# Kernel optimization log

Measured on AMD Instinct MI355X. Metric: run time of the kernel, lower is better.

## Reference

```python
import math
import jax, jax.numpy as jnp
import numpy as np

S = 2048      # seq_length
D = 1024      # embedding_dim
H = 16        # num_qkv_heads
HD = D // H   # head_size = 64
L = 4         # num_hidden_layers
V = 32000     # vocab_size
EPS = 1e-5    # nn.LayerNorm default eps


def setup_inputs() -> dict:
    key = jax.random.key(0)
    ks = jax.random.split(key, 16)
    def n(k, shape, scale=0.02):
        return (jax.random.normal(k, shape, jnp.float32) * scale)
    return {
        "input_ids": jax.random.randint(ks[0], (S,), 0, V),
        "embed":     n(ks[1], (V, D)),
        "pos_enc":   n(ks[2], (S, D)),
        # per-layer stacked params; nn.Linear stores W as [out, in]
        "wq": n(ks[3], (L, D, D)), "bq": jnp.zeros((L, D), jnp.float32),
        "wk": n(ks[4], (L, D, D)), "bk": jnp.zeros((L, D), jnp.float32),
        "wv": n(ks[5], (L, D, D)), "bv": jnp.zeros((L, D), jnp.float32),
        "wo": n(ks[6], (L, D, D)), "bo": jnp.zeros((L, D), jnp.float32),
        "ln1_g": jnp.ones((L, D), jnp.float32), "ln1_b": jnp.zeros((L, D), jnp.float32),
        "w1": n(ks[7], (L, 4 * D, D)), "b1": jnp.zeros((L, 4 * D), jnp.float32),
        "w2": n(ks[8], (L, D, 4 * D)), "b2": jnp.zeros((L, D), jnp.float32),
        "ln2_g": jnp.ones((L, D), jnp.float32), "ln2_b": jnp.zeros((L, D), jnp.float32),
        "lm_head": n(ks[9], (V, D)),
    }


def _layer_norm(x, g, b):
    mu = jnp.mean(x, axis=-1, keepdims=True)
    var = jnp.mean(jnp.square(x - mu), axis=-1, keepdims=True)
    return (x - mu) * jax.lax.rsqrt(var + EPS) * g + b


def _forward(input_ids, embed, pos_enc, wq, bq, wk, bk, wv, bv, wo, bo,
             ln1_g, ln1_b, w1, b1, w2, b2, ln2_g, ln2_b, lm_head):
    s = input_ids.shape[0]
    h = embed[input_ids] + pos_enc[:s]                      # [S, D]
    causal = jnp.tril(jnp.ones((s, s), dtype=bool))         # [S, S]
    inv_sqrt_dk = 1.0 / math.sqrt(HD)

    def layer(h, p):
        (lwq, lbq, lwk, lbk, lwv, lbv, lwo, lbo,
         g1, bn1, lw1, lb1, lw2, lb2, g2, bn2) = p
        q = (h @ lwq.T + lbq).reshape(s, H, HD).transpose(1, 0, 2)  # [H, S, HD]
        k = (h @ lwk.T + lbk).reshape(s, H, HD).transpose(1, 0, 2)
        v = (h @ lwv.T + lbv).reshape(s, H, HD).transpose(1, 0, 2)
        scores = jnp.einsum('hqd,hkd->hqk', q, k) * inv_sqrt_dk     # [H, S, S]
        scores = jnp.where(causal, scores, -jnp.inf)
        attn = jax.nn.softmax(scores, axis=-1)
        o = jnp.einsum('hqk,hkd->hqd', attn, v)                     # [H, S, HD]
        o = o.transpose(1, 0, 2).reshape(s, D) @ lwo.T + lbo        # [S, D]
        h = _layer_norm(h + o, g1, bn1)
        m = jax.nn.relu(h @ lw1.T + lb1) @ lw2.T + lb2              # [S, D]
        h = _layer_norm(h + m, g2, bn2)
        return h, None

    h, _ = jax.lax.scan(layer, h, (wq, bq, wk, bk, wv, bv, wo, bo,
                                   ln1_g, ln1_b, w1, b1, w2, b2, ln2_g, ln2_b))
    return h @ lm_head.T                                    # [S, V] logits


def reference(input_ids, embed, pos_enc, wq, bq, wk, bk, wv, bv, wo, bo,
              ln1_g, ln1_b, w1, b1, w2, b2, ln2_g, ln2_b, lm_head):
    return _forward(input_ids, embed, pos_enc, wq, bq, wk, bk, wv, bv, wo, bo,
                    ln1_g, ln1_b, w1, b1, w2, b2, ln2_g, ln2_b, lm_head)
```

## Files before the change

kernel.cpp:

```cpp
#include <hip/hip_runtime.h>
#include <hip/hip_bf16.h>

#define S 2048
#define D 1024
#define NH 16
#define HD 64
#define NL 4
#define VOCAB 32000
#define DFF 4096
#define EPS_LN 1e-5f

typedef unsigned short ushortT;
typedef __attribute__((ext_vector_type(8))) short short8;
typedef __attribute__((ext_vector_type(4))) unsigned short ushort4v;
typedef __attribute__((ext_vector_type(4))) float f32x4;

__device__ __forceinline__ ushortT f2bf(float f) {
    unsigned u = __float_as_uint(f);
    u += 0x7FFFu + ((u >> 16) & 1u);
    return (ushortT)(u >> 16);
}

__device__ __forceinline__ void gload_lds16(const ushortT* g, ushortT* l) {
    auto gp = (const __attribute__((address_space(1))) unsigned int*)(uintptr_t)g;
    auto lp = (__attribute__((address_space(3))) unsigned int*)(uintptr_t)l;
    __builtin_amdgcn_global_load_lds(gp, lp, 16, 0, 0);
}

__device__ __forceinline__ void cvt8(const float* s, ushortT* d) {
    float4 a = *(const float4*)s;
    float4 b = *(const float4*)(s + 4);
    short8 r;
    r[0] = (short)f2bf(a.x); r[1] = (short)f2bf(a.y);
    r[2] = (short)f2bf(a.z); r[3] = (short)f2bf(a.w);
    r[4] = (short)f2bf(b.x); r[5] = (short)f2bf(b.y);
    r[6] = (short)f2bf(b.z); r[7] = (short)f2bf(b.w);
    *(short8*)d = r;
}

__global__ __launch_bounds__(256) void embed_kernel(
    const int* __restrict__ ids, const float* __restrict__ embed,
    const float* __restrict__ pos, float* __restrict__ hf, ushortT* __restrict__ hb)
{
    int i = blockIdx.x * 256 + threadIdx.x;
    int srow = i >> 10;
    int d = i & (D - 1);
    float v = embed[(size_t)ids[srow] * D + d] + pos[i];
    hf[i] = v;
    hb[i] = f2bf(v);
}

__global__ __launch_bounds__(256) void convert_layer(
    const float* __restrict__ wq, const float* __restrict__ wk, const float* __restrict__ wv,
    const float* __restrict__ wo, const float* __restrict__ w1, const float* __restrict__ w2,
    const float* __restrict__ bq, const float* __restrict__ bk, const float* __restrict__ bv,
    int l, ushortT* __restrict__ wl, float* __restrict__ bqkv)
{
    constexpr int R = (D * D) / 8;
    const int u = blockIdx.x * 256 + threadIdx.x;
    if (u < 12 * R) {
        const float* src;
        if (u < 3 * R) {
            int sub = u >> 17, off = u & (R - 1);
            const float* w = (sub == 0) ? wq : (sub == 1) ? wk : wv;
            src = w + (size_t)l * D * D + (size_t)off * 8;
        } else if (u < 4 * R) {
            src = wo + (size_t)l * D * D + (size_t)(u - 3 * R) * 8;
        } else if (u < 8 * R) {
            src = w1 + (size_t)l * 4 * D * D + (size_t)(u - 4 * R) * 8;
        } else {
            src = w2 + (size_t)l * 4 * D * D + (size_t)(u - 8 * R) * 8;
        }
        cvt8(src, wl + (size_t)u * 8);
    } else if (u < 12 * R + 384) {
        int i = u - 12 * R;
        int sub = i >> 7, off = (i & 127) * 8;
        const float* src = ((sub == 0) ? bq : (sub == 1) ? bk : bv) + (size_t)l * D + off;
        *(float4*)(bqkv + sub * D + off)     = *(const float4*)src;
        *(float4*)(bqkv + sub * D + off + 4) = *(const float4*)(src + 4);
    }
}

__global__ __launch_bounds__(256) void convert_flat(
    const float* __restrict__ src, ushortT* __restrict__ dst)
{
    const size_t u = (size_t)blockIdx.x * 256 + threadIdx.x;
    cvt8(src + u * 8, dst + u * 8);
}

template<int BN, int OUTMODE, int RELU, int HASBIAS>
__global__ __launch_bounds__(256) void gemm_bf(
    const ushortT* __restrict__ A, const ushortT* __restrict__ B,
    const float* __restrict__ bias, void* __restrict__ Cn, void* __restrict__ Ct,
    int N, int K)
{
    constexpr int WN = BN / 2;
    constexpr int NCT = WN / 16;
    __shared__ alignas(16) ushortT As[128 * 32];
    __shared__ alignas(16) ushortT Bs[BN * 32];

    const int tid = threadIdx.x;
    const int id = blockIdx.x;
    const int brow = (id & 15) * 128;
    const int bcol = (id >> 4) * BN;
    const int lane = tid & 63, wid = tid >> 6;
    const int l15 = lane & 15, l4 = lane >> 4;
    const int wr = wid >> 1, wc = wid & 1;
    const int str = tid >> 2;
    const int stc = (tid & 3) * 8;

    f32x4 acc[4][NCT] = {};

    const ushortT* Ab = A + (size_t)(brow + str) * K + stc;
    const ushortT* Bb = B + (size_t)(bcol + str) * K + stc;
    ushortT* AsD = &As[tid * 8];
    ushortT* BsD = &Bs[tid * 8];

    const int nkb = K >> 5;
    for (int kb = 0; kb < nkb; ++kb) {
        const int ko = kb * 32;
        gload_lds16(Ab + ko, AsD);
        gload_lds16(Ab + ko + (size_t)64 * K, AsD + 2048);
        gload_lds16(Bb + ko, BsD);
        if (BN == 128) gload_lds16(Bb + ko + (size_t)64 * K, BsD + 2048);
        __syncthreads();

        short8 af[4], bfr[NCT];
        #pragma unroll
        for (int rt = 0; rt < 4; ++rt)
            af[rt] = *(const short8*)&As[(wr * 64 + rt * 16 + l15) * 32 + l4 * 8];
        #pragma unroll
        for (int ct = 0; ct < NCT; ++ct)
            bfr[ct] = *(const short8*)&Bs[(wc * WN + ct * 16 + l15) * 32 + l4 * 8];
        #pragma unroll
        for (int rt = 0; rt < 4; ++rt)
            #pragma unroll
            for (int ct = 0; ct < NCT; ++ct)
                acc[rt][ct] = __builtin_amdgcn_mfma_f32_16x16x32_bf16(af[rt], bfr[ct], acc[rt][ct], 0, 0, 0);
        __syncthreads();
    }

    #pragma unroll
    for (int rt = 0; rt < 4; ++rt) {
        const int crow0 = brow + wr * 64 + rt * 16 + l4 * 4;
        #pragma unroll
        for (int ct = 0; ct < NCT; ++ct) {
            const int ccol = bcol + wc * WN + ct * 16 + l15;
            const float bv = HASBIAS ? bias[ccol] : 0.0f;
            if (OUTMODE == 0) {
                float* C = (float*)Cn;
                #pragma unroll
                for (int j = 0; j < 4; ++j) {
                    float v = acc[rt][ct][j] + bv;
                    if (RELU) v = fmaxf(v, 0.0f);
                    C[(size_t)(crow0 + j) * N + ccol] = v;
                }
            } else if (OUTMODE == 1) {
                ushortT* C = (ushortT*)Cn;
                #pragma unroll
                for (int j = 0; j < 4; ++j) {
                    float v = acc[rt][ct][j] + bv;
                    if (RELU) v = fmaxf(v, 0.0f);
                    C[(size_t)(crow0 + j) * N + ccol] = f2bf(v);
                }
            }
        }
    }
}

template<int OUTMODE, int RELU, int HASBIAS>
__global__ __launch_bounds__(512) void gemm256(
    const ushortT* __restrict__ A, const ushortT* __restrict__ B,
    const float* __restrict__ bias, void* __restrict__ Cn, void* __restrict__ Ct,
    int N, int K)
{
    __shared__ alignas(128) ushortT lds[65536];

    const int tid = threadIdx.x;
    const int NB = N >> 8;
    const int bid = blockIdx.x;
    const int wgid = (bid & 7) * NB + (bid >> 3);
    const int brow = (wgid & 7) << 8;
    const int bcol = (wgid >> 3) << 8;

    const int lane = tid & 63;
    const int wid = tid >> 6;
    const int l15 = lane & 15, l4 = lane >> 4;
    const int wm = wid >> 2, wn = wid & 3;

    const int NT = K >> 6;

    const int srow = tid >> 3;
    const int scol = ((tid & 7) ^ (srow & 7)) * 8;
    const ushortT* Asrc = A + (size_t)(brow + srow) * K + scol;
    const ushortT* Bsrc = B + (size_t)(bcol + srow) * K + scol;

    auto stA = [&](int t, int h) {
        if (t < NT) {
            const int bb = t & 1;
            #pragma unroll
            for (int g = 0; g < 2; ++g)
                gload_lds16(Asrc + (size_t)(h * 128 + g * 64) * K + (size_t)t * 64,
                            &lds[bb * 32768 + h * 8192 + g * 4096 + tid * 8]);
        }
    };
    auto stB = [&](int t, int h) {
        if (t < NT) {
            const int bb = t & 1;
            #pragma unroll
            for (int g = 0; g < 2; ++g)
                gload_lds16(Bsrc + (size_t)(h * 128 + g * 64) * K + (size_t)t * 64,
                            &lds[bb * 32768 + 16384 + h * 8192 + g * 4096 + tid * 8]);
        }
    };

    f32x4 acc[2][2][4][2] = {};

    stA(0, 0); stB(0, 0); stA(0, 1); stB(0, 1); stB(1, 0); stA(1, 0);
    asm volatile("s_waitcnt vmcnt(4)" ::: "memory");
    __builtin_amdgcn_s_barrier();

#define RD_A(DST, RC)                                                          \
    _Pragma("unroll") for (int r16 = 0; r16 < 4; ++r16)                        \
    _Pragma("unroll") for (int kk = 0; kk < 2; ++kk)                           \
        DST[r16][kk] = *(const short8*)&lds[b * 32768 +                        \
            (((RC) * 128 + wm * 64 + r16 * 16 + l15) << 6) +                   \
            ((((kk << 2) + l4) ^ (l15 & 7)) << 3)];
#define RD_B(DST, CC)                                                          \
    _Pragma("unroll") for (int c16 = 0; c16 < 2; ++c16)                        \
    _Pragma("unroll") for (int kk = 0; kk < 2; ++kk)                           \
        DST[c16][kk] = *(const short8*)&lds[b * 32768 + 16384 +                \
            (((CC) * 128 + wn * 32 + c16 * 16 + l15) << 6) +                   \
            ((((kk << 2) + l4) ^ (l15 & 7)) << 3)];
#define MFMA_Q(AF, BF, RC, CC)                                                 \
    __builtin_amdgcn_s_setprio(1);                                             \
    _Pragma("unroll") for (int kk = 0; kk < 2; ++kk)                           \
    _Pragma("unroll") for (int r16 = 0; r16 < 4; ++r16)                        \
    _Pragma("unroll") for (int c16 = 0; c16 < 2; ++c16)                        \
        acc[RC][CC][r16][c16] = __builtin_amdgcn_mfma_f32_16x16x32_bf16(       \
            AF[r16][kk], BF[c16][kk], acc[RC][CC][r16][c16], 0, 0, 0);         \
    __builtin_amdgcn_s_setprio(0);
#define WAIT_LGKM asm volatile("s_waitcnt lgkmcnt(0)" ::: "memory");

    for (int t = 0; t < NT; ++t) {
        const int b = t & 1;
        short8 a_[4][2], b0[2][2], b1[2][2];

        RD_A(a_, 0); RD_B(b0, 0);
        stA(t + 1, 1);
        asm volatile("s_waitcnt lgkmcnt(8)" ::: "memory");
        __builtin_amdgcn_s_barrier();
        WAIT_LGKM;
        MFMA_Q(a_, b0, 0, 0);
        __builtin_amdgcn_s_barrier();

        RD_B(b1, 1);
        stB(t + 1, 1);
        __builtin_amdgcn_s_barrier();
        WAIT_LGKM;
        MFMA_Q(a_, b1, 0, 1);
        __builtin_amdgcn_s_barrier();

        RD_A(a_, 1);
        stB(t + 2, 0);
        __builtin_amdgcn_s_barrier();
        WAIT_LGKM;
        MFMA_Q(a_, b1, 1, 1);
        __builtin_amdgcn_s_barrier();

        stA(t + 2, 0);
        __builtin_amdgcn_s_barrier();
        MFMA_Q(a_, b0, 1, 0);
        if (t < NT - 2) { asm volatile("s_waitcnt vmcnt(4)" ::: "memory"); }
        else            { asm volatile("s_waitcnt vmcnt(0)" ::: "memory"); }
        __builtin_amdgcn_s_barrier();
    }
#undef RD_A
#undef RD_B
#undef MFMA_Q
#undef WAIT_LGKM

    #pragma unroll
    for (int rc = 0; rc < 2; ++rc)
    #pragma unroll
    for (int cc = 0; cc < 2; ++cc)
    #pragma unroll
    for (int r16 = 0; r16 < 4; ++r16)
    #pragma unroll
    for (int c16 = 0; c16 < 2; ++c16) {
        const int crow0 = brow + rc * 128 + wm * 64 + r16 * 16 + l4 * 4;
        const int ccol  = bcol + cc * 128 + wn * 32 + c16 * 16 + l15;
        const float bv = HASBIAS ? bias[ccol] : 0.0f;
        if (OUTMODE == 0) {
            float* C = (float*)Cn;
            #pragma unroll
            for (int j = 0; j < 4; ++j) {
                float v = acc[rc][cc][r16][c16][j] + bv;
                if (RELU) v = fmaxf(v, 0.0f);
                __builtin_nontemporal_store(v, &C[(size_t)(crow0 + j) * N + ccol]);
            }
        } else if (OUTMODE == 1) {
            ushortT* C = (ushortT*)Cn;
            #pragma unroll
            for (int j = 0; j < 4; ++j) {
                float v = acc[rc][cc][r16][c16][j] + bv;
                if (RELU) v = fmaxf(v, 0.0f);
                C[(size_t)(crow0 + j) * N + ccol] = f2bf(v);
            }
        }
    }
}

template<int OUTMODE, int RELU, int HASBIAS, int SWAP>
__global__ __launch_bounds__(512) void gemm256v(
    const ushortT* __restrict__ A, const ushortT* __restrict__ B,
    const float* __restrict__ bias, void* __restrict__ Cn, void* __restrict__ Ct,
    int N, int NBn, int Kloop, int stride)
{
    __shared__ alignas(128) ushortT lds[73728];

    const int tid = threadIdx.x;
    const int bid = blockIdx.x;
    const int cpx = gridDim.x >> 3;
    const int wgid = (bid & 7) * cpx + (bid >> 3);
    const int brow = (wgid & 7) << 8;
    const int rest = wgid >> 3;
    const int split = rest / NBn;
    const int bcol = (rest - split * NBn) << 7;
    const int kofs = split * Kloop;

    const int lane = tid & 63, wid = tid >> 6;
    const int l15 = lane & 15, l4 = lane >> 4;
    const int wm = wid >> 1, wn = wid & 1;
    const int NT = Kloop >> 6;

    const int srow = tid >> 3;
    const int scol = ((tid & 7) ^ (srow & 7)) * 8;
    const ushortT* Asrc = A + (size_t)(brow + srow) * stride + kofs + scol;
    const ushortT* Bsrc = B + (size_t)(bcol + srow) * stride + kofs + scol;

    auto stA = [&](int t, int h) {
        if (t < NT) {
            const int sb = t % 3;
            #pragma unroll
            for (int g = 0; g < 2; ++g)
                gload_lds16(Asrc + (size_t)(h * 128 + g * 64) * stride + (size_t)t * 64,
                            &lds[sb * 24576 + h * 8192 + g * 4096 + tid * 8]);
        }
    };
    auto stB = [&](int t) {
        if (t < NT) {
            const int sb = t % 3;
            #pragma unroll
            for (int g = 0; g < 2; ++g)
                gload_lds16(Bsrc + (size_t)(g * 64) * stride + (size_t)t * 64,
                            &lds[sb * 24576 + 16384 + g * 4096 + tid * 8]);
        }
    };

    f32x4 acc[4][4] = {};

    stA(0, 0); stA(0, 1); stB(0);
    stA(1, 0); stA(1, 1); stB(1);
    asm volatile("s_waitcnt vmcnt(6)" ::: "memory");
    __builtin_amdgcn_s_barrier();

    for (int t = 0; t < NT; ++t) {
        const unsigned abase = (unsigned)(t % 3) * 24576;
        short8 af[4][2], bf2[2][2];

        #pragma unroll
        for (int r16 = 0; r16 < 4; ++r16)
            #pragma unroll
            for (int kk = 0; kk < 2; ++kk)
                af[r16][kk] = *(const short8*)&lds[abase +
                    ((wm * 64 + r16 * 16 + l15) << 6) +
                    ((((kk << 2) + l4) ^ (l15 & 7)) << 3)];
        #pragma unroll
        for (int c16 = 0; c16 < 2; ++c16)
            #pragma unroll
            for (int kk = 0; kk < 2; ++kk)
                bf2[c16][kk] = *(const short8*)&lds[abase + 16384 +
                    ((wn * 64 + c16 * 16 + l15) << 6) +
                    ((((kk << 2) + l4) ^ (l15 & 7)) << 3)];
        stA(t + 2, 0); stA(t + 2, 1);
        asm volatile("s_waitcnt lgkmcnt(8)" ::: "memory");
        __builtin_amdgcn_s_barrier();
        asm volatile("s_waitcnt lgkmcnt(0)" ::: "memory");
        __builtin_amdgcn_s_setprio(1);
        #pragma unroll
        for (int kk = 0; kk < 2; ++kk)
            #pragma unroll
            for (int r16 = 0; r16 < 4; ++r16)
                #pragma unroll
                for (int c16 = 0; c16 < 2; ++c16)
                    acc[r16][c16] = SWAP
                        ? __builtin_amdgcn_mfma_f32_16x16x32_bf16(bf2[c16][kk], af[r16][kk], acc[r16][c16], 0, 0, 0)
                        : __builtin_amdgcn_mfma_f32_16x16x32_bf16(af[r16][kk], bf2[c16][kk], acc[r16][c16], 0, 0, 0);
        __builtin_amdgcn_s_setprio(0);
        __builtin_amdgcn_s_barrier();

        #pragma unroll
        for (int c16 = 0; c16 < 2; ++c16)
            #pragma unroll
            for (int kk = 0; kk < 2; ++kk)
                bf2[c16][kk] = *(const short8*)&lds[abase + 16384 +
                    ((wn * 64 + (c16 + 2) * 16 + l15) << 6) +
                    ((((kk << 2) + l4) ^ (l15 & 7)) << 3)];
        stB(t + 2);
        __builtin_amdgcn_s_barrier();
        asm volatile("s_waitcnt lgkmcnt(0)" ::: "memory");
        __builtin_amdgcn_s_setprio(1);
        #pragma unroll
        for (int kk = 0; kk < 2; ++kk)
            #pragma unroll
            for (int r16 = 0; r16 < 4; ++r16)
                #pragma unroll
                for (int c16 = 0; c16 < 2; ++c16)
                    acc[r16][c16 + 2] = SWAP
                        ? __builtin_amdgcn_mfma_f32_16x16x32_bf16(bf2[c16][kk], af[r16][kk], acc[r16][c16 + 2], 0, 0, 0)
                        : __builtin_amdgcn_mfma_f32_16x16x32_bf16(af[r16][kk], bf2[c16][kk], acc[r16][c16 + 2], 0, 0, 0);
        __builtin_amdgcn_s_setprio(0);
        if (t + 2 < NT) { asm volatile("s_waitcnt vmcnt(6)" ::: "memory"); }
        else            { asm volatile("s_waitcnt vmcnt(0)" ::: "memory"); }
        __builtin_amdgcn_s_barrier();
    }

    #pragma unroll
    for (int r16 = 0; r16 < 4; ++r16)
    #pragma unroll
    for (int c16 = 0; c16 < 4; ++c16) {
        if (SWAP) {
            const int row = brow + wm * 64 + r16 * 16 + l15;
            const int col = bcol + wn * 64 + c16 * 16 + l4 * 4;
            f32x4 v = acc[r16][c16];
            if (HASBIAS) {
                float4 b4 = *(const float4*)&bias[col];
                v[0] += b4.x; v[1] += b4.y; v[2] += b4.z; v[3] += b4.w;
            }
            if (RELU) {
                #pragma unroll
                for (int j = 0; j < 4; ++j) v[j] = fmaxf(v[j], 0.0f);
            }
            if (OUTMODE == 1) {
                ushort4v o;
                #pragma unroll
                for (int j = 0; j < 4; ++j) o[j] = f2bf(v[j]);
                *(ushort4v*)&((ushortT*)Cn)[(size_t)row * N + col] = o;
            } else if (OUTMODE == 3) {
                float* C = (float*)Cn + (size_t)split * 2048 * N;
                *(f32x4*)&C[(size_t)row * N + col] = v;
            } else {
                __builtin_nontemporal_store(v, (f32x4*)&((float*)Cn)[(size_t)row * N + col]);
            }
        } else {
            const int crow0 = brow + wm * 64 + r16 * 16 + l4 * 4;
            const int ccol  = bcol + wn * 64 + c16 * 16 + l15;
            const float bv = HASBIAS ? bias[ccol] : 0.0f;
            if (OUTMODE == 2) {
                if (ccol < 2048) {
                    ushortT* C = (ushortT*)Cn;
                    #pragma unroll
                    for (int j = 0; j < 4; ++j)
                        C[(size_t)(crow0 + j) * 2048 + ccol] = f2bf(acc[r16][c16][j] + bv);
                } else {
                    ushortT* C = (ushortT*)Ct;
                    ushort4v wv_;
                    #pragma unroll
                    for (int j = 0; j < 4; ++j) wv_[j] = f2bf(acc[r16][c16][j] + bv);
                    *(ushort4v*)&C[(size_t)(ccol - 2048) * S + crow0] = wv_;
                }
            } else if (OUTMODE == 1) {
                ushortT* C = (ushortT*)Cn;
                #pragma unroll
                for (int j = 0; j < 4; ++j) {
                    float v = acc[r16][c16][j] + bv;
                    if (RELU) v = fmaxf(v, 0.0f);
                    C[(size_t)(crow0 + j) * N + ccol] = f2bf(v);
                }
            } else {
                float* C = (float*)Cn;
                #pragma unroll
                for (int j = 0; j < 4; ++j) {
                    float v = acc[r16][c16][j] + bv;
                    if (RELU) v = fmaxf(v, 0.0f);
                    C[(size_t)(crow0 + j) * N + ccol] = v;
                }
            }
        }
    }
}

__global__ __launch_bounds__(256) void attn_kernel(
    const ushortT* __restrict__ qk, const ushortT* __restrict__ vt,
    ushortT* __restrict__ att)
{
    const int h = blockIdx.y;
    const int q0 = blockIdx.x * 64;
    const int tid = threadIdx.x;
    const int w = tid >> 6, lane = tid & 63;
    const int l15 = lane & 15, l4 = lane >> 4;
    const int qrow0 = q0 + w * 16;

    __shared__ short p_lds[4][16][48];

    short8 aq[2];
    {
        const ushortT* qp = qk + (size_t)(qrow0 + l15) * 2048 + h * HD + l4 * 8;
        aq[0] = *(const short8*)qp;
        aq[1] = *(const short8*)(qp + 32);
    }

    f32x4 o[4] = {};
    float lsum[4] = {0.f, 0.f, 0.f, 0.f};

    const int nkb = blockIdx.x * 2 + 2;
    for (int kb32 = 0; kb32 < nkb; ++kb32) {
        const int kb = kb32 * 32;
        f32x4 s[2] = {};
        #pragma unroll
        for (int kh = 0; kh < 2; ++kh) {
            const ushortT* kp = qk + (size_t)(kb + kh * 16 + l15) * 2048 + 1024 + h * HD + l4 * 8;
            short8 b0 = *(const short8*)kp;
            short8 b1 = *(const short8*)(kp + 32);
            s[kh] = __builtin_amdgcn_mfma_f32_16x16x32_bf16(aq[0], b0, s[kh], 0, 0, 0);
            s[kh] = __builtin_amdgcn_mfma_f32_16x16x32_bf16(aq[1], b1, s[kh], 0, 0, 0);
        }
        #pragma unroll
        for (int kh = 0; kh < 2; ++kh)
            #pragma unroll
            for (int j = 0; j < 4; ++j) {
                const int qg = qrow0 + l4 * 4 + j;
                float p = (kb + kh * 16 + l15 > qg) ? 0.0f : __expf(s[kh][j] * 0.125f);
                s[kh][j] = p;
                lsum[j] += p;
            }

        #pragma unroll
        for (int kh = 0; kh < 2; ++kh)
            #pragma unroll
            for (int j = 0; j < 4; ++j)
                p_lds[w][l4 * 4 + j][kh * 16 + l15] = (short)f2bf(s[kh][j]);
        short8 pa = *(const short8*)&p_lds[w][l15][l4 * 8];

        #pragma unroll
        for (int c = 0; c < 4; ++c) {
            short8 bv = *(const short8*)(vt + (size_t)(h * HD + c * 16 + l15) * S + kb + l4 * 8);
            o[c] = __builtin_amdgcn_mfma_f32_16x16x32_bf16(pa, bv, o[c], 0, 0, 0);
        }
    }

    float lrow[4];
    #pragma unroll
    for (int j = 0; j < 4; ++j) {
        float rs = lsum[j];
        #pragma unroll
        for (int d_ = 1; d_ < 16; d_ <<= 1) rs += __shfl_xor(rs, d_, 64);
        lrow[j] = rs;
    }

    #pragma unroll
    for (int c = 0; c < 4; ++c)
        #pragma unroll
        for (int j = 0; j < 4; ++j)
            att[(size_t)(qrow0 + l4 * 4 + j) * D + h * HD + c * 16 + l15] = f2bf(o[c][j] / lrow[j]);
}

template<int NP>
__global__ __launch_bounds__(256) void ln_kernel(
    const float* __restrict__ a,
    const float* __restrict__ p0, const float* __restrict__ p1,
    const float* __restrict__ p2, const float* __restrict__ p3,
    const float* __restrict__ pbias,
    const float* __restrict__ g, const float* __restrict__ bb,
    float* __restrict__ yf, ushortT* __restrict__ yb)
{
    const int row = blockIdx.x;
    const int tid = threadIdx.x;
    const size_t base = (size_t)row * D;
    float x[4]; float s = 0.f, s2 = 0.f;
    #pragma unroll
    for (int i = 0; i < 4; ++i) {
        const int c = tid + i * 256;
        float v = a[base + c] + p0[base + c] + pbias[c];
        if (NP > 1) v += p1[base + c] + p2[base + c] + p3[base + c];
        x[i] = v;
        s += v; s2 += v * v;
    }
    #pragma unroll
    for (int d_ = 1; d_ < 64; d_ <<= 1) {
        s  += __shfl_xor(s,  d_, 64);
        s2 += __shfl_xor(s2, d_, 64);
    }
    __shared__ float rs[4], rs2[4];
    const int wid = tid >> 6, lane = tid & 63;
    if (lane == 0) { rs[wid] = s; rs2[wid] = s2; }
    __syncthreads();
    s = rs[0] + rs[1] + rs[2] + rs[3];
    s2 = rs2[0] + rs2[1] + rs2[2] + rs2[3];
    const float mu = s * (1.0f / D);
    const float var = s2 * (1.0f / D) - mu * mu;
    const float inv = rsqrtf(var + EPS_LN);
    #pragma unroll
    for (int i = 0; i < 4; ++i) {
        const int c = tid + i * 256;
        float v = (x[i] - mu) * inv * g[c] + bb[c];
        yf[base + c] = v;
        yb[base + c] = f2bf(v);
    }
}

extern "C" void kernel_launch(void* const* d_in, const int* in_sizes, int n_in,
                              void* d_out, int out_size, void* d_ws, size_t ws_size,
                              hipStream_t stream) {
    const int*   ids   = (const int*)  d_in[0];
    const float* emb   = (const float*)d_in[1];
    const float* pos   = (const float*)d_in[2];
    const float* wq    = (const float*)d_in[3];
    const float* bq    = (const float*)d_in[4];
    const float* wk    = (const float*)d_in[5];
    const float* bk    = (const float*)d_in[6];
    const float* wv    = (const float*)d_in[7];
    const float* bv    = (const float*)d_in[8];
    const float* wo    = (const float*)d_in[9];
    const float* bo    = (const float*)d_in[10];
    const float* ln1g  = (const float*)d_in[11];
    const float* ln1b  = (const float*)d_in[12];
    const float* w1    = (const float*)d_in[13];
    const float* b1    = (const float*)d_in[14];
    const float* w2    = (const float*)d_in[15];
    const float* b2    = (const float*)d_in[16];
    const float* ln2g  = (const float*)d_in[17];
    const float* ln2b  = (const float*)d_in[18];
    const float* lmh   = (const float*)d_in[19];
    float* out = (float*)d_out;

    const size_t MB = 1024 * 1024;
    char* w = (char*)d_ws;
    float*   h_f32   = (float*)(w);
    float*   h2_f32  = (float*)(w +  8 * MB);
    float*   om2_f32 = (float*)(w + 16 * MB);
    ushortT* h_bf    = (ushortT*)(w + 24 * MB);
    ushortT* h2_bf   = (ushortT*)(w + 28 * MB);
    ushortT* qk_bf   = (ushortT*)(w + 32 * MB);
    ushortT* vt_bf   = (ushortT*)(w + 40 * MB);
    ushortT* att_bf  = (ushortT*)(w + 44 * MB);
    ushortT* m1_bf   = (ushortT*)(w + 48 * MB);
    ushortT* wl      = (ushortT*)(w + 64 * MB);
    float*   bqkv    = (float*)(w + 88 * MB);
    ushortT* lmh_bf  = (ushortT*)(w + 89 * MB);
    float*   parts   = (float*)(w + 155 * MB);

    const bool use_splitk = ws_size >= (size_t)187 * MB;

    ushortT* wqkv_bf = wl;
    ushortT* wo_bf   = wl + (size_t)3 * D * D;
    ushortT* w1_bf   = wl + (size_t)4 * D * D;
    ushortT* w2_bf   = wl + (size_t)8 * D * D;
    const size_t SD = (size_t)S * D;

    embed_kernel<<<(S * D) / 256, 256, 0, stream>>>(ids, emb, pos, h_f32, h_bf);

    for (int l = 0; l < NL; ++l) {
        convert_layer<<<6146, 256, 0, stream>>>(wq, wk, wv, wo, w1, w2, bq, bk, bv, l, wl, bqkv);

        gemm256v<2, 0, 1, 0><<<8 * 24, 512, 0, stream>>>(h_bf, wqkv_bf, bqkv, qk_bf, vt_bf,
                                                         3072, 24, D, D);

        attn_kernel<<<dim3(S / 64, NH), 256, 0, stream>>>(qk_bf, vt_bf, att_bf);

        gemm_bf<64, 0, 0, 0><<<16 * 16, 256, 0, stream>>>(att_bf, wo_bf, nullptr, om2_f32, nullptr, D, D);
        ln_kernel<1><<<S, 256, 0, stream>>>(h_f32, om2_f32, om2_f32, om2_f32, om2_f32,
                                            bo + (size_t)l * D,
                                            ln1g + (size_t)l * D, ln1b + (size_t)l * D, h2_f32, h2_bf);

        gemm256v<1, 1, 1, 1><<<8 * 32, 512, 0, stream>>>(h2_bf, w1_bf, b1 + (size_t)l * DFF, m1_bf, nullptr,
                                                         DFF, 32, D, D);

        if (use_splitk) {
            gemm256v<3, 0, 0, 1><<<8 * 8 * 4, 512, 0, stream>>>(m1_bf, w2_bf, nullptr, parts, nullptr,
                                                                D, 8, D, DFF);
            ln_kernel<4><<<S, 256, 0, stream>>>(h2_f32, parts, parts + SD, parts + 2 * SD, parts + 3 * SD,
                                                b2 + (size_t)l * D,
                                                ln2g + (size_t)l * D, ln2b + (size_t)l * D, h_f32, h_bf);
        } else {
            gemm_bf<64, 0, 0, 0><<<16 * 16, 256, 0, stream>>>(m1_bf, w2_bf, nullptr, om2_f32, nullptr, D, DFF);
            ln_kernel<1><<<S, 256, 0, stream>>>(h2_f32, om2_f32, om2_f32, om2_f32, om2_f32,
                                                b2 + (size_t)l * D,
                                                ln2g + (size_t)l * D, ln2b + (size_t)l * D, h_f32, h_bf);
        }
    }

    convert_flat<<<(VOCAB * D) / (256 * 8), 256, 0, stream>>>(lmh, lmh_bf);
    gemm256<0, 0, 0><<<8 * 125, 512, 0, stream>>>(h_bf, lmh_bf, nullptr, out, nullptr, VOCAB, D);
}
```

Baseline: 1.156 ms.

## Split attention key range across warp pairs with LDS merge, halve query tile

The attention kernel now handles 32 query rows per block instead of 64. Two warps share each 16-row query group, and each warp processes half of the causal key tiles. The partial outputs and row sums from the second warp are passed through shared memory and added in before normalisation. This doubles the grid and balances work within a block to improve occupancy and reduce per-warp serial length, at the cost of a block-level sync and extra LDS traffic. There is no running max subtraction, so summing the partial exponentials directly stays consistent with the original scheme.

```diff
diff --git a/kernel.cpp b/kernel.cpp
--- a/kernel.cpp
+++ b/kernel.cpp
@@ -496,13 +496,16 @@
     ushortT* __restrict__ att)
 {
     const int h = blockIdx.y;
-    const int q0 = blockIdx.x * 64;
+    const int qb = blockIdx.x;
+    const int q0 = qb * 32;
     const int tid = threadIdx.x;
     const int w = tid >> 6, lane = tid & 63;
+    const int r = w & 1, kh2 = w >> 1;
     const int l15 = lane & 15, l4 = lane >> 4;
-    const int qrow0 = q0 + w * 16;
+    const int qrow0 = q0 + r * 16;
 
     __shared__ short p_lds[4][16][48];
+    __shared__ alignas(16) float merge_lds[2][64][21];
 
     short8 aq[2];
     {
@@ -514,9 +517,13 @@
     f32x4 o[4] = {};
     float lsum[4] = {0.f, 0.f, 0.f, 0.f};
 
-    const int nkb = blockIdx.x * 2 + 2;
-    for (int kb32 = 0; kb32 < nkb; ++kb32) {
-        const int kb = kb32 * 32;
+    const int T  = qb + 1;
+    const int Th = (T + 1) >> 1;
+    const int t0 = kh2 ? Th : 0;
+    const int t1 = kh2 ? T : Th;
+
+    for (int tile = t0; tile < t1; ++tile) {
+        const int kb = tile * 32;
         f32x4 s[2] = {};
         #pragma unroll
         for (int kh = 0; kh < 2; ++kh) {
@@ -550,20 +557,41 @@
         }
     }
 
-    float lrow[4];
-    #pragma unroll
-    for (int j = 0; j < 4; ++j) {
-        float rs = lsum[j];
-        #pragma unroll
-        for (int d_ = 1; d_ < 16; d_ <<= 1) rs += __shfl_xor(rs, d_, 64);
-        lrow[j] = rs;
-    }
-
-    #pragma unroll
-    for (int c = 0; c < 4; ++c)
+    if (kh2 == 1) {
+        #pragma unroll
+        for (int c = 0; c < 4; ++c)
+            #pragma unroll
+            for (int j = 0; j < 4; ++j)
+                merge_lds[r][lane][c * 4 + j] = o[c][j];
         #pragma unroll
         for (int j = 0; j < 4; ++j)
-            att[(size_t)(qrow0 + l4 * 4 + j) * D + h * HD + c * 16 + l15] = f2bf(o[c][j] / lrow[j]);
+            merge_lds[r][lane][16 + j] = lsum[j];
+    }
+    __syncthreads();
+    if (kh2 == 0) {
+        #pragma unroll
+        for (int c = 0; c < 4; ++c)
+            #pragma unroll
+            for (int j = 0; j < 4; ++j)
+                o[c][j] += merge_lds[r][lane][c * 4 + j];
+        #pragma unroll
+        for (int j = 0; j < 4; ++j)
+            lsum[j] += merge_lds[r][lane][16 + j];
+
+        float lrow[4];
+        #pragma unroll
+        for (int j = 0; j < 4; ++j) {
+            float rs = lsum[j];
+            #pragma unroll
+            for (int d_ = 1; d_ < 16; d_ <<= 1) rs += __shfl_xor(rs, d_, 64);
+            lrow[j] = rs;
+        }
+        #pragma unroll
+        for (int c = 0; c < 4; ++c)
+            #pragma unroll
+            for (int j = 0; j < 4; ++j)
+                att[(size_t)(qrow0 + l4 * 4 + j) * D + h * HD + c * 16 + l15] = f2bf(o[c][j] / lrow[j]);
+    }
 }
 
 template<int NP>
@@ -667,7 +695,7 @@
         gemm256v<2, 0, 1, 0><<<8 * 24, 512, 0, stream>>>(h_bf, wqkv_bf, bqkv, qk_bf, vt_bf,
                                                          3072, 24, D, D);
 
-        attn_kernel<<<dim3(S / 64, NH), 256, 0, stream>>>(qk_bf, vt_bf, att_bf);
+        attn_kernel<<<dim3(S / 32, NH), 256, 0, stream>>>(qk_bf, vt_bf, att_bf);
 
         gemm_bf<64, 0, 0, 0><<<16 * 16, 256, 0, stream>>>(att_bf, wo_bf, nullptr, om2_f32, nullptr, D, D);
         ln_kernel<1><<<S, 256, 0, stream>>>(h_f32, om2_f32, om2_f32, om2_f32, om2_f32,
```

Result: no change. 1.159 ms (median of 2 runs) (+0.3%).
